# Optimization experiments

Measured on AMD Instinct MI355X. Metric: run time of the kernel, lower is better.

## Reference

```python
import jax, jax.numpy as jnp
import numpy as np

S, B, D, H, E, K, FF = 1024, 8, 768, 12, 8, 2, 3072


def _ln(x, w, b, eps=1e-5):
    m = x.mean(-1, keepdims=True)
    v = ((x - m) ** 2).mean(-1, keepdims=True)
    return (x - m) / jnp.sqrt(v + eps) * w + b


def setup_inputs() -> dict:
    key = jax.random.key(0)
    ks = jax.random.split(key, 12)
    s = 0.02
    return {
        "x": jax.random.normal(ks[0], (S, B, D), dtype=jnp.float32),
        "ln1_w": jnp.ones((D,), jnp.float32),
        "ln1_b": jnp.zeros((D,), jnp.float32),
        "in_proj_w": jax.random.normal(ks[1], (3 * D, D), jnp.float32) * s,
        "in_proj_b": jnp.zeros((3 * D,), jnp.float32),
        "out_proj_w": jax.random.normal(ks[2], (D, D), jnp.float32) * s,
        "out_proj_b": jnp.zeros((D,), jnp.float32),
        "ln2_w": jnp.ones((D,), jnp.float32),
        "ln2_b": jnp.zeros((D,), jnp.float32),
        "gate_w": jax.random.normal(ks[3], (E, D), jnp.float32) * s,
        "w1": jax.random.normal(ks[4], (E, D, FF), jnp.float32) * s,
        "b1": jnp.zeros((E, FF), jnp.float32),
        "w2": jax.random.normal(ks[5], (E, FF, D), jnp.float32) * s,
        "b2": jnp.zeros((E, D), jnp.float32),
    }


def reference(x, ln1_w, ln1_b, in_proj_w, in_proj_b, out_proj_w, out_proj_b,
              ln2_w, ln2_b, gate_w, w1, b1, w2, b2):
    s, b, d = x.shape
    hd = d // H
    # --- self attention (nn.MultiheadAttention, seq-first, no mask) ---
    h = _ln(x, ln1_w, ln1_b)
    qkv = h @ in_proj_w.T + in_proj_b            # [S, B, 3D]
    q, k, v = jnp.split(qkv, 3, axis=-1)

    def heads(t):
        return t.reshape(s, b, H, hd).transpose(1, 2, 0, 3)  # [B, H, S, hd]

    q, k, v = heads(q) * (hd ** -0.5), heads(k), heads(v)
    att = jax.nn.softmax(jnp.einsum('bhqd,bhkd->bhqk', q, k), axis=-1)
    o = jnp.einsum('bhqk,bhkd->bhqd', att, v).transpose(2, 0, 1, 3).reshape(s, b, d)
    o = o @ out_proj_w.T + out_proj_b
    x = x + o
    # --- MoE FFN ---
    h2 = _ln(x, ln2_w, ln2_b)
    tok = h2.reshape(-1, d)                      # [T, D], T = S*B
    logits = tok @ gate_w.T                      # [T, E]
    rw = jax.nn.softmax(logits.astype(jnp.float32), axis=-1)
    rw_top, sel = jax.lax.top_k(rw, K)           # [T, K]
    rw_top = rw_top / rw_top.sum(-1, keepdims=True)
    rw_top = rw_top.astype(tok.dtype)
    out = jnp.zeros_like(tok)
    for e in range(E):  # small fixed expert loop; math matches gather/scatter dispatch
        we = jnp.where(sel == e, rw_top, 0.0).sum(-1)       # [T] combine weight
        mid = tok @ w1[e] + b1[e]
        mid = mid * jax.nn.sigmoid(1.702 * mid)              # QuickGELU
        out = out + we[:, None] * (mid @ w2[e] + b2[e])
    return x + out.reshape(s, b, d), logits
```

## Files before the change

kernel.cpp:

```cpp
#include <hip/hip_runtime.h>
#include <stdint.h>

#define S_LEN  1024
#define BATCH  8
#define DMODEL 768
#define NHEAD  12
#define HDIM   64
#define NEXP   8
#define FFDIM  3072
#define NTOK   8192
#define D3     2304
#define NGATH  16384
#define MAXWL  80

typedef unsigned short u16;
typedef unsigned int   u32;
typedef __attribute__((ext_vector_type(8))) short bf16x8;
typedef __attribute__((ext_vector_type(4))) float f32x4;
typedef __attribute__((ext_vector_type(4))) short s16x4;

__device__ __forceinline__ u16 f2bf(float f){
  u32 x = __float_as_uint(f);
  x += 0x7fffu + ((x >> 16) & 1u);
  return (u16)(x >> 16);
}
__device__ __forceinline__ float bf2f(u16 u){
  return __uint_as_float(((u32)u) << 16);
}
__device__ __forceinline__ u32 pkbf(float a, float b){
  u32 d; asm("v_cvt_pk_bf16_f32 %0, %1, %2" : "=v"(d) : "v"(a), "v"(b)); return d;
}
__device__ __forceinline__ void gl_lds16(const void* g, void* l){
  __builtin_amdgcn_global_load_lds(
      (const __attribute__((address_space(1))) u32*)(uintptr_t)g,
      (__attribute__((address_space(3))) u32*)(u32)(uintptr_t)l,
      16, 0, 0);
}
__device__ __forceinline__ int swz64(int r){ return ((r & 7) ^ ((r >> 3) & 7)) << 4; }

__global__ __launch_bounds__(256)
void cvt_bf16(const float* __restrict__ in, u16* __restrict__ out, int n)
{
  int i = (blockIdx.x * 256 + threadIdx.x) * 4;
  if (i + 3 < n) {
    float4 v = *(const float4*)(in + i);
    out[i]     = f2bf(v.x);
    out[i + 1] = f2bf(v.y);
    out[i + 2] = f2bf(v.z);
    out[i + 3] = f2bf(v.w);
  }
}

__global__ __launch_bounds__(256)
void transpose_cvt(const float* __restrict__ in, u16* __restrict__ out, int rows, int cols)
{
  __shared__ float tile[32][33];
  const size_t eo = (size_t)blockIdx.z * rows * cols;
  in  += eo; out += eo;
  const int bx = blockIdx.x * 32, by = blockIdx.y * 32;
  const int tx = threadIdx.x, ty = threadIdx.y;
  #pragma unroll
  for (int i = 0; i < 4; i++)
    tile[ty + i * 8][tx] = in[(size_t)(by + ty + i * 8) * cols + bx + tx];
  __syncthreads();
  #pragma unroll
  for (int i = 0; i < 4; i++)
    out[(size_t)(bx + ty + i * 8) * rows + by + tx] = f2bf(tile[tx][ty + i * 8]);
}

__global__ __launch_bounds__(256)
void ln_fwd(const float* __restrict__ x, const float* __restrict__ w, const float* __restrict__ b,
            u16* __restrict__ out)
{
  const int t = blockIdx.x, tid = threadIdx.x;
  const float* xr = x + (size_t)t * DMODEL;
  const float v0 = xr[tid], v1 = xr[tid + 256], v2 = xr[tid + 512];
  float s = v0 + v1 + v2, ss = v0 * v0 + v1 * v1 + v2 * v2;
  #pragma unroll
  for (int d = 1; d < 64; d <<= 1) { s += __shfl_xor(s, d); ss += __shfl_xor(ss, d); }
  __shared__ float rs[4], rq[4];
  if ((tid & 63) == 0) { rs[tid >> 6] = s; rq[tid >> 6] = ss; }
  __syncthreads();
  s  = rs[0] + rs[1] + rs[2] + rs[3];
  ss = rq[0] + rq[1] + rq[2] + rq[3];
  const float mean = s * (1.f / DMODEL);
  const float rstd = rsqrtf(ss * (1.f / DMODEL) - mean * mean + 1e-5f);
  u16* orow = out + (size_t)t * DMODEL;
  orow[tid]       = f2bf((v0 - mean) * rstd * w[tid]       + b[tid]);
  orow[tid + 256] = f2bf((v1 - mean) * rstd * w[tid + 256] + b[tid + 256]);
  orow[tid + 512] = f2bf((v2 - mean) * rstd * w[tid + 512] + b[tid + 512]);
}

__global__ __launch_bounds__(256)
void ln2_gate(const float* __restrict__ x1, const float* __restrict__ w, const float* __restrict__ b,
              const float* __restrict__ gate_w, u16* __restrict__ h2,
              float* __restrict__ logits, float* __restrict__ selw, int* __restrict__ seli)
{
  const int t = blockIdx.x, tid = threadIdx.x;
  const float* xr = x1 + (size_t)t * DMODEL;
  const float v0 = xr[tid], v1 = xr[tid + 256], v2 = xr[tid + 512];
  float s = v0 + v1 + v2, ss = v0 * v0 + v1 * v1 + v2 * v2;
  #pragma unroll
  for (int d = 1; d < 64; d <<= 1) { s += __shfl_xor(s, d); ss += __shfl_xor(ss, d); }
  __shared__ float rs[4], rq[4];
  if ((tid & 63) == 0) { rs[tid >> 6] = s; rq[tid >> 6] = ss; }
  __syncthreads();
  s  = rs[0] + rs[1] + rs[2] + rs[3];
  ss = rq[0] + rq[1] + rq[2] + rq[3];
  const float mean = s * (1.f / DMODEL);
  const float rstd = rsqrtf(ss * (1.f / DMODEL) - mean * mean + 1e-5f);
  __shared__ float row[DMODEL];
  const float y0 = (v0 - mean) * rstd * w[tid]       + b[tid];
  const float y1 = (v1 - mean) * rstd * w[tid + 256] + b[tid + 256];
  const float y2 = (v2 - mean) * rstd * w[tid + 512] + b[tid + 512];
  row[tid] = y0; row[tid + 256] = y1; row[tid + 512] = y2;
  u16* hr = h2 + (size_t)t * DMODEL;
  hr[tid] = f2bf(y0); hr[tid + 256] = f2bf(y1); hr[tid + 512] = f2bf(y2);
  __syncthreads();
  __shared__ float lg[NEXP];
  if (tid < 64) {
    const int e = tid >> 3, j = tid & 7;
    const float* gw = gate_w + e * DMODEL;
    float a = 0.f;
    for (int d = j; d < DMODEL; d += 8) a += row[d] * gw[d];
    a += __shfl_xor(a, 1); a += __shfl_xor(a, 2); a += __shfl_xor(a, 4);
    if (j == 0) lg[e] = a;
  }
  __syncthreads();
  if (tid < NEXP) logits[(size_t)t * NEXP + tid] = lg[tid];
  if (tid == 0) {
    int ia = 0, ib = -1;
    float va = -1e30f, vb = -1e30f;
    #pragma unroll
    for (int e = 0; e < NEXP; e++) {
      const float p = lg[e];
      if (p > va)      { vb = va; ib = ia; va = p; ia = e; }
      else if (p > vb) { vb = p; ib = e; }
    }
    const float pb = __expf(vb - va);
    const float inv = 1.f / (1.f + pb);
    selw[2 * t]     = inv;
    selw[2 * t + 1] = pb * inv;
    seli[2 * t]     = ia;
    seli[2 * t + 1] = ib;
  }
}

__global__ __launch_bounds__(256)
void route_count(const int* __restrict__ seli, int* __restrict__ blkcnt)
{
  __shared__ int c[NEXP];
  const int tid = threadIdx.x;
  if (tid < NEXP) c[tid] = 0;
  __syncthreads();
  const int t = blockIdx.x * 256 + tid;
  atomicAdd(&c[seli[2 * t]], 1);
  atomicAdd(&c[seli[2 * t + 1]], 1);
  __syncthreads();
  if (tid < NEXP) blkcnt[blockIdx.x * NEXP + tid] = c[tid];
}

__global__ void route_scan(const int* __restrict__ blkcnt, int* __restrict__ offs,
                           int* __restrict__ blkbase, int* __restrict__ wl, int* __restrict__ nwork)
{
  const int tid = threadIdx.x;
  __shared__ int tot[NEXP];
  __shared__ int off_s[NEXP + 1];
  if (tid < NEXP) {
    int s = 0;
    for (int blk = 0; blk < 32; blk++) s += blkcnt[blk * NEXP + tid];
    tot[tid] = s;
  }
  __syncthreads();
  if (tid == 0) {
    int run = 0;
    for (int e = 0; e < NEXP; e++) { off_s[e] = run; run += tot[e]; }
    off_s[NEXP] = run;
    int nw = 0;
    for (int e = 0; e < NEXP; e++) {
      const int nb = (tot[e] + 255) >> 8;
      for (int i2 = 0; i2 < nb; i2++) wl[nw++] = (e << 16) | i2;
    }
    nwork[0] = nw;
  }
  __syncthreads();
  if (tid <= NEXP) offs[tid] = off_s[tid];
  if (tid < NEXP) {
    int run = off_s[tid];
    for (int blk = 0; blk < 32; blk++) { blkbase[blk * NEXP + tid] = run; run += blkcnt[blk * NEXP + tid]; }
  }
}

__global__ __launch_bounds__(256)
void route_place(const int* __restrict__ seli, const int* __restrict__ blkbase,
                 int* __restrict__ perm, int* __restrict__ posmap)
{
  __shared__ int cnts[2][4][NEXP];
  __shared__ int base[NEXP];
  const int tid = threadIdx.x, l = tid & 63, w = tid >> 6, blk = blockIdx.x;
  const int t = blk * 256 + tid;
  const unsigned long long ltm = (1ull << l) - 1ull;
  int my_e[2], my_r[2];
  my_e[0] = seli[2 * t]; my_e[1] = seli[2 * t + 1];
  my_r[0] = 0; my_r[1] = 0;
  if (tid < NEXP) base[tid] = blkbase[blk * NEXP + tid];
  #pragma unroll
  for (int k = 0; k < 2; k++) {
    #pragma unroll
    for (int ee = 0; ee < NEXP; ee++) {
      const unsigned long long msk = __ballot(my_e[k] == ee);
      if (my_e[k] == ee) my_r[k] = (int)__popcll(msk & ltm);
      if (l == ee) cnts[k][w][ee] = (int)__popcll(msk);
    }
  }
  __syncthreads();
  #pragma unroll
  for (int k = 0; k < 2; k++) {
    const int e = my_e[k];
    int pre = base[e];
    for (int k2 = 0; k2 < 2; k2++)
      for (int w2 = 0; w2 < 4; w2++)
        if (k2 < k || (k2 == k && w2 < w)) pre += cnts[k2][w2][e];
    const int pos = pre + my_r[k];
    perm[pos] = t;
    posmap[2 * t + k] = pos;
  }
}

template<int MODE>
__global__ __launch_bounds__(512, 2)
void gemm256(const u16* __restrict__ A, const u16* __restrict__ Bw,
             int M, int N, int Kd,
             const float* __restrict__ bias,
             void* __restrict__ outp,
             const int* __restrict__ perm, const int* __restrict__ offs,
             const int* __restrict__ wl, const int* __restrict__ nwork)
{
  extern __shared__ u16 smem[];
  const int tid = threadIdx.x;
  const int l   = tid & 63;
  const int w   = tid >> 6;
  const int wm  = w >> 2, wn = w & 3;
  const int bn  = blockIdx.y;

  int gbase = 0, cnt = M, e = 0, bm = blockIdx.x;
  if (MODE >= 2) {
    if (blockIdx.x >= nwork[0]) return;
    const int wk = wl[blockIdx.x];
    e  = wk >> 16;
    bm = wk & 0xffff;
    gbase = offs[e];
    cnt   = offs[e + 1] - gbase;
  }
  const u16*   Bp = Bw   + (MODE >= 2 ? (size_t)e * N * Kd : 0);
  const float* bp = bias + (MODE >= 2 ? e * N : 0);

  int arow[4], acol[4], brow[4];
  #pragma unroll
  for (int i = 0; i < 4; i++) {
    const int c = tid + 512 * i;
    const int r = c >> 3;
    const int f = (r & 7) ^ ((r >> 3) & 7);
    acol[i] = ((c & 7) ^ f) * 8;
    brow[i] = bn * 256 + r;
    int g;
    if (MODE == 2)      { int gp = gbase + bm * 256 + r; if (gp > NGATH - 1) gp = NGATH - 1; g = perm[gp]; }
    else if (MODE == 3) { int gp = gbase + bm * 256 + r; if (gp > NGATH - 1) gp = NGATH - 1; g = gp; }
    else                g = bm * 256 + r;
    arow[i] = g;
  }

  f32x4 acc[8][4] = {};
  const int nk = Kd >> 6;

  #pragma unroll
  for (int i = 0; i < 4; i++) {
    gl_lds16(A  + (size_t)arow[i] * Kd + acol[i], &smem[(tid + 512 * i) * 8]);
    gl_lds16(Bp + (size_t)brow[i] * Kd + acol[i], &smem[32768 + (tid + 512 * i) * 8]);
  }

  int cur = 0;
  for (int kt = 0; kt < nk; kt++) {
    const bool pf = (kt + 1 < nk);
    if (pf) {
      const int kb = (kt + 1) * 64;
      u16* Anx = smem + (cur ^ 1) * 16384;
      u16* Bnx = smem + 32768 + (cur ^ 1) * 16384;
      #pragma unroll
      for (int i = 0; i < 4; i++) {
        gl_lds16(A  + (size_t)arow[i] * Kd + kb + acol[i], &Anx[(tid + 512 * i) * 8]);
        gl_lds16(Bp + (size_t)brow[i] * Kd + kb + acol[i], &Bnx[(tid + 512 * i) * 8]);
      }
      asm volatile("s_waitcnt vmcnt(8)" ::: "memory");
    } else {
      asm volatile("s_waitcnt vmcnt(0)" ::: "memory");
    }
    __builtin_amdgcn_s_barrier();
    __builtin_amdgcn_sched_barrier(0);

    const char* Ac = (const char*)(smem + cur * 16384);
    const char* Bc = (const char*)(smem + 32768 + cur * 16384);
    #pragma unroll
    for (int ks = 0; ks < 2; ks++) {
      bf16x8 bv[4];
      #pragma unroll
      for (int n = 0; n < 4; n++) {
        const int row = wn * 64 + n * 16 + (l & 15);
        bv[n] = *(const bf16x8*)(Bc + ((row * 128 + ks * 64 + (l >> 4) * 16) ^ swz64(row)));
      }
      #pragma unroll
      for (int m = 0; m < 8; m++) {
        const int row = wm * 128 + m * 16 + (l & 15);
        const bf16x8 af = *(const bf16x8*)(Ac + ((row * 128 + ks * 64 + (l >> 4) * 16) ^ swz64(row)));
        #pragma unroll
        for (int n = 0; n < 4; n++)
          acc[m][n] = __builtin_amdgcn_mfma_f32_16x16x32_bf16(bv[n], af, acc[m][n], 0, 0, 0);
      }
    }
    if (pf) __builtin_amdgcn_s_barrier();
    cur ^= 1;
  }

  f32x4 biasv[4];
  int   c0[4];
  #pragma unroll
  for (int n = 0; n < 4; n++) {
    c0[n] = bn * 256 + wn * 64 + n * 16 + ((l >> 4) << 2);
    biasv[n] = *(const f32x4*)(bp + c0[n]);
  }
  #pragma unroll
  for (int m = 0; m < 8; m++) {
    const int row = bm * 256 + wm * 128 + m * 16 + (l & 15);
    #pragma unroll
    for (int n = 0; n < 4; n++) {
      f32x4 v = acc[m][n] + biasv[n];
      if (MODE == 0) {
        *(uint2*)((u16*)outp + (size_t)row * N + c0[n]) =
            make_uint2(pkbf(v[0], v[1]), pkbf(v[2], v[3]));
      } else if (MODE == 2) {
        if (row < cnt) {
          #pragma unroll
          for (int r = 0; r < 4; r++)
            v[r] = v[r] * __builtin_amdgcn_rcpf(1.f + __expf(-1.702f * v[r]));
          *(uint2*)((u16*)outp + (size_t)(gbase + row) * FFDIM + c0[n]) =
              make_uint2(pkbf(v[0], v[1]), pkbf(v[2], v[3]));
        }
      } else {
        if (row < cnt)
          *(uint2*)((u16*)outp + (size_t)(gbase + row) * DMODEL + c0[n]) =
              make_uint2(pkbf(v[0], v[1]), pkbf(v[2], v[3]));
      }
    }
  }
}

__global__ __launch_bounds__(256)
void gemm128_op(const u16* __restrict__ A, const u16* __restrict__ Bw,
                int M, int N, int Kd,
                const float* __restrict__ bias, const float* __restrict__ resid,
                float* __restrict__ outp)
{
  __shared__ u16 As[2][128 * 64];
  __shared__ u16 Bs[2][128 * 64];
  const int tid = threadIdx.x;
  const int l   = tid & 63;
  const int w   = tid >> 6;
  const int wm  = w >> 1, wn = w & 1;
  const int bn  = blockIdx.y, bm = blockIdx.x;

  int arow[4], acol[4], brow[4];
  #pragma unroll
  for (int i = 0; i < 4; i++) {
    const int c = tid + 256 * i;
    const int r = c >> 3;
    const int f = (r & 7) ^ ((r >> 3) & 7);
    acol[i] = ((c & 7) ^ f) * 8;
    brow[i] = bn * 128 + r;
    arow[i] = bm * 128 + r;
  }

  f32x4 acc[4][4] = {};
  const int nk = Kd >> 6;
  #pragma unroll
  for (int i = 0; i < 4; i++) {
    gl_lds16(A  + (size_t)arow[i] * Kd + acol[i], &As[0][(i * 256 + w * 64) * 8]);
    gl_lds16(Bw + (size_t)brow[i] * Kd + acol[i], &Bs[0][(i * 256 + w * 64) * 8]);
  }
  int cur = 0;
  for (int kt = 0; kt < nk; kt++) {
    const bool pf = (kt + 1 < nk);
    if (pf) {
      const int kb = (kt + 1) * 64;
      #pragma unroll
      for (int i = 0; i < 4; i++) {
        gl_lds16(A  + (size_t)arow[i] * Kd + kb + acol[i], &As[cur ^ 1][(i * 256 + w * 64) * 8]);
        gl_lds16(Bw + (size_t)brow[i] * Kd + kb + acol[i], &Bs[cur ^ 1][(i * 256 + w * 64) * 8]);
      }
      asm volatile("s_waitcnt vmcnt(8)" ::: "memory");
    } else {
      asm volatile("s_waitcnt vmcnt(0)" ::: "memory");
    }
    __builtin_amdgcn_s_barrier();
    __builtin_amdgcn_sched_barrier(0);
    #pragma unroll
    for (int ks = 0; ks < 2; ks++) {
      bf16x8 af[4], bv[4];
      #pragma unroll
      for (int m = 0; m < 4; m++) {
        const int row = wm * 64 + m * 16 + (l & 15);
        af[m] = *(const bf16x8*)((const char*)&As[cur][0] +
                  ((row * 128 + ks * 64 + (l >> 4) * 16) ^ swz64(row)));
      }
      #pragma unroll
      for (int n = 0; n < 4; n++) {
        const int row = wn * 64 + n * 16 + (l & 15);
        bv[n] = *(const bf16x8*)((const char*)&Bs[cur][0] +
                  ((row * 128 + ks * 64 + (l >> 4) * 16) ^ swz64(row)));
      }
      #pragma unroll
      for (int m = 0; m < 4; m++)
        #pragma unroll
        for (int n = 0; n < 4; n++)
          acc[m][n] = __builtin_amdgcn_mfma_f32_16x16x32_bf16(bv[n], af[m], acc[m][n], 0, 0, 0);
    }
    if (pf) __builtin_amdgcn_s_barrier();
    cur ^= 1;
  }

  f32x4 biasv[4];
  int   c0[4];
  #pragma unroll
  for (int n = 0; n < 4; n++) {
    c0[n] = bn * 128 + wn * 64 + n * 16 + ((l >> 4) << 2);
    biasv[n] = *(const f32x4*)(bias + c0[n]);
  }
  #pragma unroll
  for (int m = 0; m < 4; m++) {
    const int row = bm * 128 + wm * 64 + m * 16 + (l & 15);
    #pragma unroll
    for (int n = 0; n < 4; n++) {
      const size_t o = (size_t)row * N + c0[n];
      f32x4 v = acc[m][n] + biasv[n] + *(const f32x4*)(resid + o);
      *(f32x4*)(outp + o) = v;
    }
  }
}

__global__ __launch_bounds__(256)
void attn_fwd(const u16* __restrict__ qkv, u16* __restrict__ o)
{
  __shared__ u16 Ksw[64 * 64];
  __shared__ u16 Vt [64 * 64];
  __shared__ u16 Pl [4 * 16 * 64];
  const int tid = threadIdx.x;
  const int l   = tid & 63, w = tid >> 6;
  const int qt  = blockIdx.x;
  const int b_  = blockIdx.y / NHEAD;
  const int hh  = blockIdx.y % NHEAD;

  const int qrow = qt * 64 + w * 16 + (l & 15);
  const size_t qoff = ((size_t)(qrow * BATCH + b_)) * D3 + hh * HDIM + (l >> 4) * 8;
  const bf16x8 qa0 = *(const bf16x8*)&qkv[qoff];
  const bf16x8 qa1 = *(const bf16x8*)&qkv[qoff + 32];

  f32x4 oacc[4] = {};
  float m_[4], l_[4];
  #pragma unroll
  for (int r = 0; r < 4; r++) { m_[r] = -1e30f; l_[r] = 0.f; }

  u16* Pw = Pl + w * 1024;
  const int pswz = swz64(l & 15);

  for (int kt = 0; kt < 16; kt++) {
    #pragma unroll
    for (int i = 0; i < 2; i++) {
      const int c = tid + 256 * i;
      const int key = c >> 3, dimb = (c & 7) * 8;
      const size_t gb = ((size_t)((kt * 64 + key) * BATCH + b_)) * D3 + hh * HDIM + dimb;
      const bf16x8 kd = *(const bf16x8*)&qkv[gb + DMODEL];
      const bf16x8 vd = *(const bf16x8*)&qkv[gb + 2 * DMODEL];
      *(bf16x8*)((char*)Ksw + ((key * 128 + dimb * 2) ^ swz64(key))) = kd;
      #pragma unroll
      for (int j = 0; j < 8; j++) {
        const int dim = dimb + j;
        *(u16*)((char*)Vt + ((dim * 128 + key * 2) ^ swz64(dim))) = (u16)vd[j];
      }
    }
    __syncthreads();

    f32x4 sc[4] = {};
    #pragma unroll
    for (int kb2 = 0; kb2 < 4; kb2++) {
      const int key = kb2 * 16 + (l & 15);
      const int ksz = swz64(key);
      #pragma unroll
      for (int ks = 0; ks < 2; ks++) {
        const bf16x8 kf = *(const bf16x8*)((char*)Ksw +
            ((key * 128 + (ks * 32 + (l >> 4) * 8) * 2) ^ ksz));
        sc[kb2] = __builtin_amdgcn_mfma_f32_16x16x32_bf16(ks ? qa1 : qa0, kf, sc[kb2], 0, 0, 0);
      }
    }
    #pragma unroll
    for (int kb2 = 0; kb2 < 4; kb2++)
      #pragma unroll
      for (int r = 0; r < 4; r++) sc[kb2][r] *= 0.125f;

    float nm[4], corr[4], ps[4];
    #pragma unroll
    for (int r = 0; r < 4; r++) {
      float pm = fmaxf(fmaxf(sc[0][r], sc[1][r]), fmaxf(sc[2][r], sc[3][r]));
      pm = fmaxf(pm, __shfl_xor(pm, 1));
      pm = fmaxf(pm, __shfl_xor(pm, 2));
      pm = fmaxf(pm, __shfl_xor(pm, 4));
      pm = fmaxf(pm, __shfl_xor(pm, 8));
      nm[r]   = fmaxf(m_[r], pm);
      corr[r] = __expf(m_[r] - nm[r]);
      m_[r]   = nm[r];
      ps[r]   = 0.f;
    }
    #pragma unroll
    for (int kb2 = 0; kb2 < 4; kb2++) {
      #pragma unroll
      for (int r = 0; r < 4; r++) {
        const float p = __expf(sc[kb2][r] - nm[r]);
        ps[r] += p;
        const int prow = (l >> 4) * 4 + r;
        const int pcol = kb2 * 16 + (l & 15);
        *(u16*)((char*)Pw + ((prow * 128 + pcol * 2) ^ swz64(prow))) = f2bf(p);
      }
    }
    #pragma unroll
    for (int r = 0; r < 4; r++) {
      float s = ps[r];
      s += __shfl_xor(s, 1); s += __shfl_xor(s, 2);
      s += __shfl_xor(s, 4); s += __shfl_xor(s, 8);
      l_[r] = l_[r] * corr[r] + s;
      #pragma unroll
      for (int ob = 0; ob < 4; ob++) oacc[ob][r] *= corr[r];
    }

    #pragma unroll
    for (int ob = 0; ob < 4; ob++) {
      const int dim = ob * 16 + (l & 15);
      const int vsz = swz64(dim);
      #pragma unroll
      for (int ks = 0; ks < 2; ks++) {
        const int kko = (ks * 32 + (l >> 4) * 8) * 2;
        const bf16x8 pf = *(const bf16x8*)((char*)Pw + (((l & 15) * 128 + kko) ^ pswz));
        const bf16x8 vf = *(const bf16x8*)((char*)Vt + ((dim * 128 + kko) ^ vsz));
        oacc[ob] = __builtin_amdgcn_mfma_f32_16x16x32_bf16(pf, vf, oacc[ob], 0, 0, 0);
      }
    }
    __syncthreads();
  }

  #pragma unroll
  for (int r = 0; r < 4; r++) {
    const float inv = 1.f / l_[r];
    const int qs = qt * 64 + w * 16 + (l >> 4) * 4 + r;
    #pragma unroll
    for (int ob = 0; ob < 4; ob++)
      o[((size_t)(qs * BATCH + b_)) * DMODEL + hh * HDIM + ob * 16 + (l & 15)] =
          f2bf(oacc[ob][r] * inv);
  }
}

__global__ __launch_bounds__(192)
void moe_combine(const float* __restrict__ x1, const u16* __restrict__ eout,
                 const int* __restrict__ posmap, const float* __restrict__ selw,
                 float* __restrict__ out)
{
  const int t = blockIdx.x, j = threadIdx.x;
  const int p0 = posmap[2 * t], p1 = posmap[2 * t + 1];
  const float w0 = selw[2 * t], w1 = selw[2 * t + 1];
  const float4 xv = ((const float4*)(x1 + (size_t)t * DMODEL))[j];
  const s16x4 a = ((const s16x4*)(eout + (size_t)p0 * DMODEL))[j];
  const s16x4 c = ((const s16x4*)(eout + (size_t)p1 * DMODEL))[j];
  float4 r;
  r.x = xv.x + w0 * bf2f((u16)a[0]) + w1 * bf2f((u16)c[0]);
  r.y = xv.y + w0 * bf2f((u16)a[1]) + w1 * bf2f((u16)c[1]);
  r.z = xv.z + w0 * bf2f((u16)a[2]) + w1 * bf2f((u16)c[2]);
  r.w = xv.w + w0 * bf2f((u16)a[3]) + w1 * bf2f((u16)c[3]);
  ((float4*)(out + (size_t)t * DMODEL))[j] = r;
}

#define MB (1ull << 20)
static const size_t OFF_H    = 0;
static const size_t OFF_QKV  = 16 * MB;
static const size_t OFF_O    = 54 * MB;
static const size_t OFF_IPW  = 67 * MB;
static const size_t OFF_OPW  = 71 * MB;
static const size_t OFF_MID  = 0;
static const size_t OFF_X1   = 101 * MB;
static const size_t OFF_H2   = 127 * MB;
static const size_t OFF_W1T  = 140 * MB;
static const size_t OFF_W2T  = 178 * MB;
static const size_t OFF_EOUT = 216 * MB;
static const size_t OFF_SELW = 242 * MB;
static const size_t OFF_PERM = 242 * MB + (1 << 16);
static const size_t OFF_POS  = 242 * MB + (2 << 16);
static const size_t OFF_SELI = 242 * MB + (3 << 16);
static const size_t OFF_BCNT = 242 * MB + (4 << 16);
static const size_t OFF_BBASE= 242 * MB + (4 << 16) + 4096;
static const size_t OFF_OFFS = 242 * MB + (4 << 16) + 8192;
static const size_t OFF_WL   = 242 * MB + (5 << 16);
static const size_t OFF_NW   = 242 * MB + (5 << 16) + 1024;

extern "C" void kernel_launch(void* const* d_in, const int* in_sizes, int n_in,
                              void* d_out, int out_size, void* d_ws, size_t ws_size,
                              hipStream_t stream)
{
  const float* x     = (const float*)d_in[0];
  const float* ln1w  = (const float*)d_in[1];
  const float* ln1b  = (const float*)d_in[2];
  const float* ipw_f = (const float*)d_in[3];
  const float* ipb   = (const float*)d_in[4];
  const float* opw_f = (const float*)d_in[5];
  const float* opb   = (const float*)d_in[6];
  const float* ln2w  = (const float*)d_in[7];
  const float* ln2b  = (const float*)d_in[8];
  const float* gatew = (const float*)d_in[9];
  const float* w1    = (const float*)d_in[10];
  const float* b1    = (const float*)d_in[11];
  const float* w2    = (const float*)d_in[12];
  const float* b2    = (const float*)d_in[13];

  char* ws = (char*)d_ws;
  u16*   h    = (u16*)(ws + OFF_H);
  u16*   qkv  = (u16*)(ws + OFF_QKV);
  u16*   ob   = (u16*)(ws + OFF_O);
  u16*   ipw  = (u16*)(ws + OFF_IPW);
  u16*   opw  = (u16*)(ws + OFF_OPW);
  u16*   mid  = (u16*)(ws + OFF_MID);
  float* x1   = (float*)(ws + OFF_X1);
  u16*   h2   = (u16*)(ws + OFF_H2);
  u16*   w1t  = (u16*)(ws + OFF_W1T);
  u16*   w2t  = (u16*)(ws + OFF_W2T);
  u16*   eout = (u16*)(ws + OFF_EOUT);
  float* selw = (float*)(ws + OFF_SELW);
  int*   perm = (int*)(ws + OFF_PERM);
  int*   posm = (int*)(ws + OFF_POS);
  int*   seli = (int*)(ws + OFF_SELI);
  int*   bcnt = (int*)(ws + OFF_BCNT);
  int*   bbas = (int*)(ws + OFF_BBASE);
  int*   offs = (int*)(ws + OFF_OFFS);
  int*   wl   = (int*)(ws + OFF_WL);
  int*   nwork= (int*)(ws + OFF_NW);
  float* outx  = (float*)d_out;
  float* outlg = outx + (size_t)NTOK * DMODEL;

  static const int LDS_BYTES = 131072;
  (void)hipFuncSetAttribute((const void*)gemm256<0>, hipFuncAttributeMaxDynamicSharedMemorySize, LDS_BYTES);
  (void)hipFuncSetAttribute((const void*)gemm256<2>, hipFuncAttributeMaxDynamicSharedMemorySize, LDS_BYTES);
  (void)hipFuncSetAttribute((const void*)gemm256<3>, hipFuncAttributeMaxDynamicSharedMemorySize, LDS_BYTES);

  cvt_bf16<<<(D3 * DMODEL) / 1024, 256, 0, stream>>>(ipw_f, ipw, D3 * DMODEL);
  cvt_bf16<<<(DMODEL * DMODEL) / 1024, 256, 0, stream>>>(opw_f, opw, DMODEL * DMODEL);
  transpose_cvt<<<dim3(FFDIM / 32, DMODEL / 32, NEXP), dim3(32, 8), 0, stream>>>(w1, w1t, DMODEL, FFDIM);
  transpose_cvt<<<dim3(DMODEL / 32, FFDIM / 32, NEXP), dim3(32, 8), 0, stream>>>(w2, w2t, FFDIM, DMODEL);

  ln_fwd<<<NTOK, 256, 0, stream>>>(x, ln1w, ln1b, h);
  gemm256<0><<<dim3(NTOK / 256, D3 / 256, 1), 512, LDS_BYTES, stream>>>(
      h, ipw, NTOK, D3, DMODEL, ipb, qkv, nullptr, nullptr, nullptr, nullptr);
  attn_fwd<<<dim3(S_LEN / 64, BATCH * NHEAD), 256, 0, stream>>>(qkv, ob);
  gemm128_op<<<dim3(NTOK / 128, DMODEL / 128, 1), 256, 0, stream>>>(
      ob, opw, NTOK, DMODEL, DMODEL, opb, x, x1);

  ln2_gate<<<NTOK, 256, 0, stream>>>(x1, ln2w, ln2b, gatew, h2, outlg, selw, seli);
  route_count<<<32, 256, 0, stream>>>(seli, bcnt);
  route_scan<<<1, 64, 0, stream>>>(bcnt, offs, bbas, wl, nwork);
  route_place<<<32, 256, 0, stream>>>(seli, bbas, perm, posm);

  gemm256<2><<<dim3(MAXWL, FFDIM / 256, 1), 512, LDS_BYTES, stream>>>(
      h2, w1t, NGATH, FFDIM, DMODEL, b1, mid, perm, offs, wl, nwork);
  gemm256<3><<<dim3(MAXWL, DMODEL / 256, 1), 512, LDS_BYTES, stream>>>(
      mid, w2t, NGATH, DMODEL, FFDIM, b2, eout, nullptr, offs, wl, nwork);

  moe_combine<<<NTOK, 192, 0, stream>>>(x1, eout, posm, selw, outx);
}
```

Before: 559.0 us.

## Interleave global-to-LDS prefetch chunks with MFMA phases in GEMM main loop

Splits each K-tile iteration of the shared GEMM kernel into four MFMA phases. The global-to-LDS prefetch of the next tile is issued one quarter at a time between those phases rather than all at once at the top of the iteration. LDS offsets are precomputed once, MFMA blocks run at raised wave priority via s_setprio, and the shared-memory layout changes to interleave the A and B buffers per stage. The aim is to hide global load latency behind matrix math and to smooth memory issue. In exchange it adds several extra workgroup barriers per K step.

```diff
diff --git a/kernel.cpp b/kernel.cpp
--- a/kernel.cpp
+++ b/kernel.cpp
@@ -273,51 +273,118 @@
   f32x4 acc[8][4] = {};
   const int nk = Kd >> 6;
 
+  int aoff[8], boff[4];
+  #pragma unroll
+  for (int m = 0; m < 8; m++) {
+    const int row = wm * 128 + m * 16 + (l & 15);
+    aoff[m] = (row * 128 + (l >> 4) * 16) ^ swz64(row);
+  }
+  #pragma unroll
+  for (int n = 0; n < 4; n++) {
+    const int row = wn * 64 + n * 16 + (l & 15);
+    boff[n] = (row * 128 + (l >> 4) * 16) ^ swz64(row);
+  }
+
   #pragma unroll
   for (int i = 0; i < 4; i++) {
     gl_lds16(A  + (size_t)arow[i] * Kd + acol[i], &smem[(tid + 512 * i) * 8]);
-    gl_lds16(Bp + (size_t)brow[i] * Kd + acol[i], &smem[32768 + (tid + 512 * i) * 8]);
+    gl_lds16(Bp + (size_t)brow[i] * Kd + acol[i], &smem[16384 + (tid + 512 * i) * 8]);
   }
 
   int cur = 0;
   for (int kt = 0; kt < nk; kt++) {
     const bool pf = (kt + 1 < nk);
+    const int  kb = (kt + 1) * 64;
+    u16* nA = smem + (cur ^ 1) * 32768;
+    u16* nB = nA + 16384;
+    const char* Ac = (const char*)(smem + cur * 32768);
+    const char* Bc = (const char*)(smem + cur * 32768 + 16384);
+    bf16x8 bv[4], af[4];
+
     if (pf) {
-      const int kb = (kt + 1) * 64;
-      u16* Anx = smem + (cur ^ 1) * 16384;
-      u16* Bnx = smem + 32768 + (cur ^ 1) * 16384;
-      #pragma unroll
-      for (int i = 0; i < 4; i++) {
-        gl_lds16(A  + (size_t)arow[i] * Kd + kb + acol[i], &Anx[(tid + 512 * i) * 8]);
-        gl_lds16(Bp + (size_t)brow[i] * Kd + kb + acol[i], &Bnx[(tid + 512 * i) * 8]);
-      }
-      asm volatile("s_waitcnt vmcnt(8)" ::: "memory");
+      gl_lds16(A  + (size_t)arow[0] * Kd + kb + acol[0], &nA[tid * 8]);
+      gl_lds16(Bp + (size_t)brow[0] * Kd + kb + acol[0], &nB[tid * 8]);
+      asm volatile("s_waitcnt vmcnt(2)" ::: "memory");
     } else {
       asm volatile("s_waitcnt vmcnt(0)" ::: "memory");
     }
     __builtin_amdgcn_s_barrier();
     __builtin_amdgcn_sched_barrier(0);
-
-    const char* Ac = (const char*)(smem + cur * 16384);
-    const char* Bc = (const char*)(smem + 32768 + cur * 16384);
-    #pragma unroll
-    for (int ks = 0; ks < 2; ks++) {
-      bf16x8 bv[4];
-      #pragma unroll
-      for (int n = 0; n < 4; n++) {
-        const int row = wn * 64 + n * 16 + (l & 15);
-        bv[n] = *(const bf16x8*)(Bc + ((row * 128 + ks * 64 + (l >> 4) * 16) ^ swz64(row)));
-      }
-      #pragma unroll
-      for (int m = 0; m < 8; m++) {
-        const int row = wm * 128 + m * 16 + (l & 15);
-        const bf16x8 af = *(const bf16x8*)(Ac + ((row * 128 + ks * 64 + (l >> 4) * 16) ^ swz64(row)));
-        #pragma unroll
-        for (int n = 0; n < 4; n++)
-          acc[m][n] = __builtin_amdgcn_mfma_f32_16x16x32_bf16(bv[n], af, acc[m][n], 0, 0, 0);
-      }
-    }
-    if (pf) __builtin_amdgcn_s_barrier();
+    #pragma unroll
+    for (int n = 0; n < 4; n++) bv[n] = *(const bf16x8*)(Bc + boff[n]);
+    #pragma unroll
+    for (int m = 0; m < 4; m++) af[m] = *(const bf16x8*)(Ac + aoff[m]);
+    asm volatile("s_waitcnt lgkmcnt(0)" ::: "memory");
+    __builtin_amdgcn_sched_barrier(0);
+    __builtin_amdgcn_s_setprio(1);
+    #pragma unroll
+    for (int m = 0; m < 4; m++)
+      #pragma unroll
+      for (int n = 0; n < 4; n++)
+        acc[m][n] = __builtin_amdgcn_mfma_f32_16x16x32_bf16(bv[n], af[m], acc[m][n], 0, 0, 0);
+    __builtin_amdgcn_s_setprio(0);
+    __builtin_amdgcn_s_barrier();
+    __builtin_amdgcn_sched_barrier(0);
+
+    #pragma unroll
+    for (int m = 0; m < 4; m++) af[m] = *(const bf16x8*)(Ac + aoff[m + 4]);
+    if (pf) {
+      gl_lds16(A  + (size_t)arow[1] * Kd + kb + acol[1], &nA[(tid + 512) * 8]);
+      gl_lds16(Bp + (size_t)brow[1] * Kd + kb + acol[1], &nB[(tid + 512) * 8]);
+    }
+    __builtin_amdgcn_s_barrier();
+    asm volatile("s_waitcnt lgkmcnt(0)" ::: "memory");
+    __builtin_amdgcn_sched_barrier(0);
+    __builtin_amdgcn_s_setprio(1);
+    #pragma unroll
+    for (int m = 0; m < 4; m++)
+      #pragma unroll
+      for (int n = 0; n < 4; n++)
+        acc[m + 4][n] = __builtin_amdgcn_mfma_f32_16x16x32_bf16(bv[n], af[m], acc[m + 4][n], 0, 0, 0);
+    __builtin_amdgcn_s_setprio(0);
+    __builtin_amdgcn_s_barrier();
+    __builtin_amdgcn_sched_barrier(0);
+
+    #pragma unroll
+    for (int n = 0; n < 4; n++) bv[n] = *(const bf16x8*)(Bc + (boff[n] ^ 64));
+    #pragma unroll
+    for (int m = 0; m < 4; m++) af[m] = *(const bf16x8*)(Ac + (aoff[m] ^ 64));
+    if (pf) {
+      gl_lds16(A  + (size_t)arow[2] * Kd + kb + acol[2], &nA[(tid + 1024) * 8]);
+      gl_lds16(Bp + (size_t)brow[2] * Kd + kb + acol[2], &nB[(tid + 1024) * 8]);
+    }
+    __builtin_amdgcn_s_barrier();
+    asm volatile("s_waitcnt lgkmcnt(0)" ::: "memory");
+    __builtin_amdgcn_sched_barrier(0);
+    __builtin_amdgcn_s_setprio(1);
+    #pragma unroll
+    for (int m = 0; m < 4; m++)
+      #pragma unroll
+      for (int n = 0; n < 4; n++)
+        acc[m][n] = __builtin_amdgcn_mfma_f32_16x16x32_bf16(bv[n], af[m], acc[m][n], 0, 0, 0);
+    __builtin_amdgcn_s_setprio(0);
+    __builtin_amdgcn_s_barrier();
+    __builtin_amdgcn_sched_barrier(0);
+
+    #pragma unroll
+    for (int m = 0; m < 4; m++) af[m] = *(const bf16x8*)(Ac + (aoff[m + 4] ^ 64));
+    if (pf) {
+      gl_lds16(A  + (size_t)arow[3] * Kd + kb + acol[3], &nA[(tid + 1536) * 8]);
+      gl_lds16(Bp + (size_t)brow[3] * Kd + kb + acol[3], &nB[(tid + 1536) * 8]);
+    }
+    __builtin_amdgcn_s_barrier();
+    asm volatile("s_waitcnt lgkmcnt(0)" ::: "memory");
+    __builtin_amdgcn_sched_barrier(0);
+    __builtin_amdgcn_s_setprio(1);
+    #pragma unroll
+    for (int m = 0; m < 4; m++)
+      #pragma unroll
+      for (int n = 0; n < 4; n++)
+        acc[m + 4][n] = __builtin_amdgcn_mfma_f32_16x16x32_bf16(bv[n], af[m], acc[m + 4][n], 0, 0, 0);
+    __builtin_amdgcn_s_setprio(0);
+    __builtin_amdgcn_s_barrier();
+    __builtin_amdgcn_sched_barrier(0);
+
     cur ^= 1;
   }
 
```

Result: no change. 560.2 us (+0.2%).
